# Performance work log

Hardware: AMD Instinct MI355X
Metric: run time of the kernel (lower is better)

Reference implementation:

```python
import jax, jax.numpy as jnp
import numpy as np

EMBED_DIM = 1024
N_TOKENS = 8192


def setup_inputs() -> dict:
    key = jax.random.key(0)
    kx, kr, ke = jax.random.split(key, 3)
    x = jax.random.normal(kx, (N_TOKENS, EMBED_DIM), dtype=jnp.float32)
    rotation_params = jax.random.normal(kr, (EMBED_DIM * EMBED_DIM,), dtype=jnp.float32) * 0.02
    entangle_params = jax.random.normal(ke, (EMBED_DIM * EMBED_DIM,), dtype=jnp.float32) * 0.02
    return {"x": x, "rotation_params": rotation_params, "entangle_params": entangle_params}


def reference(x, rotation_params, entangle_params):
    d = EMBED_DIM
    w_q = rotation_params.reshape(d, d)
    w_k = entangle_params.reshape(d, d)
    q = x @ w_q                      # [N, D]
    k = x @ w_k                      # [N, D]
    v = x                            # v is the raw input (as in source)
    scale = 1.0 / np.sqrt(d).astype(np.float32)
    scores = jax.nn.softmax(jnp.einsum('nd,md->nm', q, k) * scale, axis=-1)  # [N, N]
    return scores @ v                # [N, D]
```

## Files before the change

### kernel.cpp

```cpp
#include <hip/hip_runtime.h>
#include <hip/hip_bf16.h>
#include <stdint.h>

#define EMBED 1024
#define NTOK 8192
#define QRANGE 4.5f

#define BUFB (48 * 1024)
#define SMEM_TOTAL (3 * BUFB)
#define BBUF (64 * 1024)
#define SMEM_BIG (2 * BBUF)

typedef short bf16x8 __attribute__((ext_vector_type(8)));
typedef float f32x4 __attribute__((ext_vector_type(4)));
typedef int int4v __attribute__((ext_vector_type(4)));

__device__ inline unsigned short f2bf(float f) {
    union { float f; unsigned u; } c; c.f = f;
    unsigned u = c.u;
    unsigned r = (u + 0x7fffu + ((u >> 16) & 1u)) >> 16;
    return (unsigned short)r;
}

__device__ __forceinline__ void bar_sync_drain() {
    asm volatile("s_waitcnt vmcnt(0)\n\ts_barrier" ::: "memory");
}
__device__ __forceinline__ void bar_sync_cnt6() {
    asm volatile("s_waitcnt vmcnt(6)\n\ts_barrier" ::: "memory");
}

__device__ inline void xcd_remap(int& bx, int& by) {
    if ((gridDim.y & 7) == 0) {
        int bid = by * gridDim.x + bx;
        by = bid % gridDim.y;
        bx = bid / gridDim.y;
    }
}

__global__ void prep_x(const float* __restrict__ x, unsigned short* __restrict__ xb,
                       unsigned short* __restrict__ xbT) {
    __shared__ unsigned short tile[32][33];
    int bj = blockIdx.x, bi = blockIdx.y;
    int tx = threadIdx.x, ty = threadIdx.y;
#pragma unroll
    for (int r = 0; r < 4; ++r) {
        int row = ty + r * 8;
        size_t gi = (size_t)(bi * 32 + row) * EMBED + bj * 32 + tx;
        unsigned short h = f2bf(x[gi]);
        xb[gi] = h;
        tile[row][tx] = h;
    }
    __syncthreads();
#pragma unroll
    for (int r = 0; r < 4; ++r) {
        int row = ty + r * 8;
        xbT[(size_t)(bj * 32 + row) * NTOK + bi * 32 + tx] = tile[tx][row];
    }
}

__global__ void prep_w2(const float* __restrict__ wq, const float* __restrict__ wk,
                        unsigned short* __restrict__ wT, float* __restrict__ Z) {
    if (blockIdx.z == 2) {
        if (blockIdx.x == 0 && blockIdx.y == 0) {
            int t = threadIdx.y * 32 + threadIdx.x;
            for (int i = t; i < NTOK; i += 256) Z[i] = 0.f;
        }
        return;
    }
    __shared__ unsigned short tile[32][33];
    int bj = blockIdx.x, bi = blockIdx.y;
    int tx = threadIdx.x, ty = threadIdx.y;
    const float* w = blockIdx.z ? wk : wq;
    unsigned short* dst = wT + (size_t)blockIdx.z * EMBED * EMBED;
#pragma unroll
    for (int r = 0; r < 4; ++r) {
        int row = ty + r * 8;
        tile[row][tx] = f2bf(w[(size_t)(bi * 32 + row) * EMBED + bj * 32 + tx]);
    }
    __syncthreads();
#pragma unroll
    for (int r = 0; r < 4; ++r) {
        int row = ty + r * 8;
        dst[(size_t)(bj * 32 + row) * EMBED + bi * 32 + tx] = tile[tx][row];
    }
}

template<int MODE> struct GAcc { using T = f32x4; };
template<> struct GAcc<1> { using T = int4v; };
template<int MODE> struct GFrag { using T = bf16x8; };
template<> struct GFrag<1> { using T = int4v; };

__device__ __forceinline__ void stage_rows(const char* __restrict__ G, char* dst,
                                           size_t base, int ld, int kB, int tid,
                                           int niter) {
    const int srow = tid >> 3;
    const int csw  = ((tid & 7) ^ (srow & 7)) << 4;
    const int dof  = srow * 128 + ((tid & 7) << 4);
    const char* g = G + (base + srow) * (size_t)ld + kB + csw;
    char* d = dst + dof;
    for (int it = 0; it < niter; ++it)
        __builtin_amdgcn_global_load_lds(
            (const __attribute__((address_space(1))) void*)(g + (size_t)it * 64 * ld),
            (__attribute__((address_space(3))) void*)(d + it * 64 * 128), 16, 0, 0);
}

__device__ __forceinline__ void stage256(const char* __restrict__ A,
                                         const char* __restrict__ B,
                                         char* dst, size_t aBase, size_t bBase,
                                         int ldA, int ldB, int kB, int tid) {
    stage_rows(A, dst, aBase, ldA, kB, tid, 4);
    stage_rows(B, dst + 32768, bBase, ldB, kB, tid, 2);
}

__device__ __forceinline__ void stage_big(const char* __restrict__ A,
                                          const char* __restrict__ B,
                                          char* dst, size_t aBase, size_t bBase,
                                          int ldA, int ldB, int kB, int tid) {
    stage_rows(A, dst, aBase, ldA, kB, tid, 4);
    stage_rows(B, dst + 32768, bBase, ldB, kB, tid, 4);
}

template<int MODE, int NF>
__device__ __forceinline__ void ld_fr(typename GFrag<MODE>::T (&fr)[NF],
                                      const char* S, int wbase, int l15, int quad,
                                      int s) {
    using FT = typename GFrag<MODE>::T;
    const int sl = ((((s << 2) + quad) ^ (l15 & 7)) << 4);
#pragma unroll
    for (int f = 0; f < NF; ++f)
        fr[f] = *(const FT*)(S + (wbase + f * 16 + l15) * 128 + sl);
}

template<int MODE, int MT, int NT>
__device__ __forceinline__ void mfma_mn(typename GAcc<MODE>::T (&acc)[MT][NT],
                                        typename GFrag<MODE>::T (&af)[MT],
                                        typename GFrag<MODE>::T (&bf)[NT]) {
#pragma unroll
    for (int mt = 0; mt < MT; ++mt)
#pragma unroll
        for (int nt = 0; nt < NT; ++nt) {
            if constexpr (MODE == 1)
                acc[mt][nt] = __builtin_amdgcn_mfma_i32_16x16x64_i8(
                    af[mt], bf[nt], acc[mt][nt], 0, 0, 0);
            else
                acc[mt][nt] = __builtin_amdgcn_mfma_f32_16x16x32_bf16(
                    af[mt], bf[nt], acc[mt][nt], 0, 0, 0);
        }
}

template<int MODE>
__global__ __launch_bounds__(512, 2) void gemm256(
    const char* __restrict__ A, const char* __restrict__ B, void* __restrict__ Cv,
    int KB, int ldA, int ldB, int ldC, float qsc,
    float* __restrict__ Z, int beta, const float* __restrict__ Zn)
{
    extern __shared__ char smem[];
    const int tid  = threadIdx.x;
    const int lane = tid & 63;
    const int wid  = tid >> 6;
    const int wm   = (wid >> 1) << 6;
    const int wn   = (wid & 1) << 6;
    const int quad = lane >> 4;
    const int l15  = lane & 15;

    int bx = blockIdx.x, by = blockIdx.y;
    xcd_remap(bx, by);
    const size_t mBase = (size_t)by * 256;
    const size_t nBase = (size_t)bx * 128;

    using FT = typename GFrag<MODE>::T;
    typename GAcc<MODE>::T acc[4][4] = {};
    FT a0[4], b0[4], a1[4], b1[4];

    const int nsteps = KB >> 7;
    stage256(A, B, smem, mBase, nBase, ldA, ldB, 0, tid);
    if (nsteps > 1) {
        stage256(A, B, smem + BUFB, mBase, nBase, ldA, ldB, 128, tid);
        bar_sync_cnt6();
    } else {
        bar_sync_drain();
    }
    __builtin_amdgcn_sched_barrier(0);
    ld_fr<MODE, 4>(a0, smem, wm, l15, quad, 0);
    ld_fr<MODE, 4>(b0, smem + 32768, wn, l15, quad, 0);

    int bc = 0;
    for (int t = 0; t < nsteps; ++t) {
        const char* As = smem + bc * BUFB;
        ld_fr<MODE, 4>(a1, As, wm, l15, quad, 1);
        ld_fr<MODE, 4>(b1, As + 32768, wn, l15, quad, 1);
        __builtin_amdgcn_s_setprio(1);
        mfma_mn<MODE, 4, 4>(acc, a0, b0);
        __builtin_amdgcn_s_setprio(0);
        if (t + 1 < nsteps) {
            bar_sync_drain();
            __builtin_amdgcn_sched_barrier(0);
            int bn = bc + 1; if (bn >= 3) bn -= 3;
            const char* An = smem + bn * BUFB;
            ld_fr<MODE, 4>(a0, An, wm, l15, quad, 0);
            ld_fr<MODE, 4>(b0, An + 32768, wn, l15, quad, 0);
            if (t + 2 < nsteps) {
                int bs = bc + 2; if (bs >= 3) bs -= 3;
                stage256(A, B, smem + bs * BUFB, mBase, nBase, ldA, ldB,
                         (t + 2) << 7, tid);
            }
        }
        __builtin_amdgcn_s_setprio(1);
        mfma_mn<MODE, 4, 4>(acc, a1, b1);
        __builtin_amdgcn_s_setprio(0);
        ++bc; if (bc >= 3) bc -= 3;
    }
    __syncthreads();

    if constexpr (MODE == 2) {
        float* stf = (float*)smem + wid * (16 * 68);
        float* C = (float*)Cv;
#pragma unroll
        for (int mt = 0; mt < 4; ++mt) {
#pragma unroll
            for (int nt = 0; nt < 4; ++nt) {
                f32x4 v = acc[mt][nt];
#pragma unroll
                for (int r = 0; r < 4; ++r)
                    stf[(quad * 4 + r) * 68 + nt * 16 + l15] = v[r];
            }
#pragma unroll
            for (int pass = 0; pass < 4; ++pass) {
                int row = pass * 4 + (lane >> 4);
                int cc  = (lane & 15) * 4;
                f32x4 vv = *(const f32x4*)(stf + row * 68 + cc);
                size_t grow = mBase + wm + mt * 16 + row;
                float* gp = C + grow * (size_t)ldC + nBase + wn + cc;
                if (beta) {
                    f32x4 old = *(const f32x4*)gp;
                    vv = vv + old;
                }
                if (Zn) {
                    float inv = 1.0f / Zn[grow];
                    vv = vv * inv;
                }
                *(f32x4*)gp = vv;
            }
        }
    }
}

template<int MODE>
__global__ __launch_bounds__(512, 2) void gemmBig(
    const char* __restrict__ A, const char* __restrict__ B, void* __restrict__ Cv,
    int KB, int ldA, int ldB, int ldC, float qsc, float* __restrict__ Z)
{
    extern __shared__ char smem[];
    const int tid  = threadIdx.x;
    const int lane = tid & 63;
    const int wid  = tid >> 6;
    const int wm   = (wid >> 2) << 7;
    const int wn   = (wid & 3) << 6;
    const int quad = lane >> 4;
    const int l15  = lane & 15;

    int bx = blockIdx.x, by = blockIdx.y;
    xcd_remap(bx, by);
    const size_t mBase = (size_t)by * 256;
    const size_t nBase = (size_t)bx * 256;

    using FT = typename GFrag<MODE>::T;
    typename GAcc<MODE>::T acc[8][4] = {};
    FT af[8], bf[4];

    const int nsteps = KB >> 7;
    stage_big(A, B, smem, mBase, nBase, ldA, ldB, 0, tid);

    for (int t = 0; t < nsteps; ++t) {
        bar_sync_drain();
        __builtin_amdgcn_sched_barrier(0);
        if (t + 1 < nsteps)
            stage_big(A, B, smem + ((t + 1) & 1) * BBUF, mBase, nBase, ldA, ldB,
                      (t + 1) << 7, tid);
        const char* As = smem + (t & 1) * BBUF;
        const char* Bs = As + 32768;
#pragma unroll
        for (int s = 0; s < 2; ++s) {
            ld_fr<MODE, 8>(af, As, wm, l15, quad, s);
            ld_fr<MODE, 4>(bf, Bs, wn, l15, quad, s);
            __builtin_amdgcn_s_setprio(1);
            mfma_mn<MODE, 8, 4>(acc, af, bf);
            __builtin_amdgcn_s_setprio(0);
        }
    }
    __syncthreads();

    if constexpr (MODE == 0) {
        float* stf = (float*)smem + wid * (16 * 68);
        unsigned char* C = (unsigned char*)Cv;
        const float qinv = 127.0f / QRANGE;
#pragma unroll
        for (int mt = 0; mt < 8; ++mt) {
#pragma unroll
            for (int nt = 0; nt < 4; ++nt) {
                f32x4 v = acc[mt][nt];
#pragma unroll
                for (int r = 0; r < 4; ++r)
                    stf[(quad * 4 + r) * 68 + nt * 16 + l15] = v[r];
            }
#pragma unroll
            for (int pass = 0; pass < 4; ++pass) {
                int row = pass * 4 + (lane >> 4);
                int cc  = (lane & 15) * 4;
                f32x4 vv = *(const f32x4*)(stf + row * 68 + cc);
                int b[4];
#pragma unroll
                for (int r = 0; r < 4; ++r)
                    b[r] = __float2int_rn(fminf(fmaxf(vv[r] * qinv, -127.f), 127.f));
                int pk = (b[0] & 0xff) | ((b[1] & 0xff) << 8) |
                         ((b[2] & 0xff) << 16) | (b[3] << 24);
                size_t grow = mBase + wm + mt * 16 + row;
                *(int*)(C + grow * (size_t)ldC + nBase + wn + cc) = pk;
            }
        }
    } else {
        unsigned short* st = (unsigned short*)smem + wid * (16 * 72);
        unsigned short* C = (unsigned short*)Cv;
#pragma unroll
        for (int mt = 0; mt < 8; ++mt) {
            float rs[4] = {0.f, 0.f, 0.f, 0.f};
#pragma unroll
            for (int nt = 0; nt < 4; ++nt) {
                int4v v = acc[mt][nt];
#pragma unroll
                for (int r = 0; r < 4; ++r) {
                    float e = __expf((float)v[r] * qsc);
                    rs[r] += e;
                    st[(quad * 4 + r) * 72 + nt * 16 + l15] = f2bf(e);
                }
            }
#pragma unroll
            for (int r = 0; r < 4; ++r) {
                float s = rs[r];
                s += __shfl_xor(s, 1);
                s += __shfl_xor(s, 2);
                s += __shfl_xor(s, 4);
                s += __shfl_xor(s, 8);
                if (l15 == 0)
                    atomicAdd(&Z[mBase + wm + mt * 16 + quad * 4 + r], s);
            }
#pragma unroll
            for (int pass = 0; pass < 2; ++pass) {
                int row = pass * 8 + (lane >> 3);
                int cc  = (lane & 7) * 8;
                bf16x8 vv = *(const bf16x8*)(st + row * 72 + cc);
                size_t grow = mBase + wm + mt * 16 + row;
                *(bf16x8*)(C + grow * (size_t)ldC + nBase + wn + cc) = vv;
            }
        }
    }
}

extern "C" void kernel_launch(void* const* d_in, const int* in_sizes, int n_in,
                              void* d_out, int out_size, void* d_ws, size_t ws_size,
                              hipStream_t stream) {
    const float* x  = (const float*)d_in[0];
    const float* wq = (const float*)d_in[1];
    const float* wk = (const float*)d_in[2];
    float* out = (float*)d_out;

    char* p = (char*)d_ws;
    unsigned short* xb   = (unsigned short*)p; p += (size_t)NTOK * EMBED * 2;
    unsigned short* xbT  = (unsigned short*)p; p += (size_t)NTOK * EMBED * 2;
    signed char*    qk8  = (signed char*)p;    p += (size_t)NTOK * 2 * EMBED;
    unsigned short* wqkT = (unsigned short*)p; p += (size_t)2 * EMBED * EMBED * 2;
    float* Z = (float*)p; p += (size_t)NTOK * 4;
    unsigned short* P = (unsigned short*)p;

    size_t used  = (size_t)(p - (char*)d_ws);
    size_t avail = ws_size > used ? (ws_size - used) / 2 : 0;
    int NC = NTOK;
    while (NC > 256 && (size_t)NTOK * NC > avail) NC >>= 1;

    hipFuncSetAttribute((const void*)gemm256<2>,
                        hipFuncAttributeMaxDynamicSharedMemorySize, SMEM_TOTAL);
    hipFuncSetAttribute((const void*)gemmBig<0>,
                        hipFuncAttributeMaxDynamicSharedMemorySize, SMEM_BIG);
    hipFuncSetAttribute((const void*)gemmBig<1>,
                        hipFuncAttributeMaxDynamicSharedMemorySize, SMEM_BIG);

    prep_x<<<dim3(EMBED / 32, NTOK / 32), dim3(32, 8), 0, stream>>>(x, xb, xbT);
    prep_w2<<<dim3(32, 32, 3), dim3(32, 8), 0, stream>>>(wq, wk, wqkT, Z);

    gemmBig<0><<<dim3(2 * EMBED / 256, NTOK / 256), 512, SMEM_BIG, stream>>>(
        (const char*)xb, (const char*)wqkT, qk8,
        2 * EMBED, 2 * EMBED, 2 * EMBED, 2 * EMBED,
        0.f, nullptr);

    const char* q8 = (const char*)qk8;
    const char* k8 = q8 + EMBED;
    const float qsc = (QRANGE / 127.0f) * (QRANGE / 127.0f) / 32.0f;
    for (int c0 = 0; c0 < NTOK; c0 += NC) {
        const bool last = (c0 + NC >= NTOK);
        gemmBig<1><<<dim3(NC / 256, NTOK / 256), 512, SMEM_BIG, stream>>>(
            q8, k8 + (size_t)c0 * 2 * EMBED, P,
            EMBED, 2 * EMBED, 2 * EMBED, NC,
            qsc, Z);
        gemm256<2><<<dim3(EMBED / 128, NTOK / 256), 512, SMEM_TOTAL, stream>>>(
            (const char*)P, (const char*)(xbT + c0), out,
            NC * 2, NC * 2, NTOK * 2, EMBED,
            0.f, nullptr, c0 > 0 ? 1 : 0, last ? Z : nullptr);
    }
}
```

Before: 338.0 us.

## Quantize softmax probabilities and V to int8 for the PV GEMM

The second GEMM (P @ V) now runs on int8 MFMA instead of bf16. The unnormalized exp scores are stored as int8 centered at PMAX/2, V is stored transposed as int8, and a per-column V rowsum correction restores the offset in the epilogue. This halves the P and V traffic and uses the faster int8 matrix instructions. The cost is much coarser quantization of probabilities, which are clamped at PMAX, so accuracy may drift.

```diff
diff --git a/kernel.cpp b/kernel.cpp
--- a/kernel.cpp
+++ b/kernel.cpp
@@ -4,7 +4,10 @@
 
 #define EMBED 1024
 #define NTOK 8192
-#define QRANGE 4.5f
+#define XR 4.5f
+#define QKR 3.8f
+#define PMAX 14.0f
+#define PC (PMAX * 0.5f)
 
 #define BUFB (48 * 1024)
 #define SMEM_TOTAL (3 * BUFB)
@@ -38,23 +41,25 @@
 }
 
 __global__ void prep_x(const float* __restrict__ x, unsigned short* __restrict__ xb,
-                       unsigned short* __restrict__ xbT) {
-    __shared__ unsigned short tile[32][33];
+                       signed char* __restrict__ x8T) {
+    __shared__ signed char tile8[32][33];
     int bj = blockIdx.x, bi = blockIdx.y;
     int tx = threadIdx.x, ty = threadIdx.y;
+    const float qinv = 127.0f / XR;
 #pragma unroll
     for (int r = 0; r < 4; ++r) {
         int row = ty + r * 8;
         size_t gi = (size_t)(bi * 32 + row) * EMBED + bj * 32 + tx;
-        unsigned short h = f2bf(x[gi]);
-        xb[gi] = h;
-        tile[row][tx] = h;
+        float v = x[gi];
+        xb[gi] = f2bf(v);
+        tile8[row][tx] = (signed char)__float2int_rn(
+            fminf(fmaxf(v * qinv, -127.f), 127.f));
     }
     __syncthreads();
 #pragma unroll
     for (int r = 0; r < 4; ++r) {
         int row = ty + r * 8;
-        xbT[(size_t)(bj * 32 + row) * NTOK + bi * 32 + tx] = tile[tx][row];
+        x8T[(size_t)(bj * 32 + row) * NTOK + bi * 32 + tx] = tile8[tx][row];
     }
 }
 
@@ -85,10 +90,28 @@
     }
 }
 
+__global__ void rowsum8(const signed char* __restrict__ x8T, int* __restrict__ S8,
+                        int c0, int NC) {
+    int d = blockIdx.x * 4 + (threadIdx.x >> 6);
+    int lane = threadIdx.x & 63;
+    const signed char* r = x8T + (size_t)d * NTOK + c0;
+    int s = 0;
+    for (int i = lane * 4; i < NC; i += 256) {
+        int w = *(const int*)(r + i);
+        s += (int)(signed char)(w & 0xff) + (int)(signed char)((w >> 8) & 0xff)
+           + (int)(signed char)((w >> 16) & 0xff) + (int)(signed char)((w >> 24) & 0xff);
+    }
+    s += __shfl_xor(s, 1);  s += __shfl_xor(s, 2);  s += __shfl_xor(s, 4);
+    s += __shfl_xor(s, 8);  s += __shfl_xor(s, 16); s += __shfl_xor(s, 32);
+    if (lane == 0) S8[d] = s;
+}
+
 template<int MODE> struct GAcc { using T = f32x4; };
 template<> struct GAcc<1> { using T = int4v; };
+template<> struct GAcc<3> { using T = int4v; };
 template<int MODE> struct GFrag { using T = bf16x8; };
 template<> struct GFrag<1> { using T = int4v; };
+template<> struct GFrag<3> { using T = int4v; };
 
 __device__ __forceinline__ void stage_rows(const char* __restrict__ G, char* dst,
                                            size_t base, int ld, int kB, int tid,
@@ -139,7 +162,7 @@
     for (int mt = 0; mt < MT; ++mt)
 #pragma unroll
         for (int nt = 0; nt < NT; ++nt) {
-            if constexpr (MODE == 1)
+            if constexpr (MODE == 1 || MODE == 3)
                 acc[mt][nt] = __builtin_amdgcn_mfma_i32_16x16x64_i8(
                     af[mt], bf[nt], acc[mt][nt], 0, 0, 0);
             else
@@ -152,7 +175,8 @@
 __global__ __launch_bounds__(512, 2) void gemm256(
     const char* __restrict__ A, const char* __restrict__ B, void* __restrict__ Cv,
     int KB, int ldA, int ldB, int ldC, float qsc,
-    float* __restrict__ Z, int beta, const float* __restrict__ Zn)
+    float* __restrict__ Z, int beta, const float* __restrict__ Zn,
+    const int* __restrict__ S8c, float ccoef)
 {
     extern __shared__ char smem[];
     const int tid  = threadIdx.x;
@@ -212,17 +236,28 @@
     }
     __syncthreads();
 
-    if constexpr (MODE == 2) {
+    if constexpr (MODE == 2 || MODE == 3) {
         float* stf = (float*)smem + wid * (16 * 68);
         float* C = (float*)Cv;
+        float scorr[4] = {0.f, 0.f, 0.f, 0.f};
+        if constexpr (MODE == 3) {
+#pragma unroll
+            for (int nt = 0; nt < 4; ++nt)
+                scorr[nt] = ccoef * (float)S8c[nBase + wn + nt * 16 + l15];
+        }
 #pragma unroll
         for (int mt = 0; mt < 4; ++mt) {
 #pragma unroll
             for (int nt = 0; nt < 4; ++nt) {
-                f32x4 v = acc[mt][nt];
-#pragma unroll
-                for (int r = 0; r < 4; ++r)
-                    stf[(quad * 4 + r) * 68 + nt * 16 + l15] = v[r];
+#pragma unroll
+                for (int r = 0; r < 4; ++r) {
+                    float fv;
+                    if constexpr (MODE == 3)
+                        fv = (float)acc[mt][nt][r] * qsc + scorr[nt];
+                    else
+                        fv = acc[mt][nt][r];
+                    stf[(quad * 4 + r) * 68 + nt * 16 + l15] = fv;
+                }
             }
 #pragma unroll
             for (int pass = 0; pass < 4; ++pass) {
@@ -293,7 +328,7 @@
     if constexpr (MODE == 0) {
         float* stf = (float*)smem + wid * (16 * 68);
         unsigned char* C = (unsigned char*)Cv;
-        const float qinv = 127.0f / QRANGE;
+        const float qinv = 127.0f / QKR;
 #pragma unroll
         for (int mt = 0; mt < 8; ++mt) {
 #pragma unroll
@@ -319,8 +354,9 @@
             }
         }
     } else {
-        unsigned short* st = (unsigned short*)smem + wid * (16 * 72);
-        unsigned short* C = (unsigned short*)Cv;
+        float* stf = (float*)smem + wid * (16 * 68);
+        unsigned char* C = (unsigned char*)Cv;
+        const float qinv = 254.0f / PMAX;
 #pragma unroll
         for (int mt = 0; mt < 8; ++mt) {
             float rs[4] = {0.f, 0.f, 0.f, 0.f};
@@ -331,7 +367,7 @@
                 for (int r = 0; r < 4; ++r) {
                     float e = __expf((float)v[r] * qsc);
                     rs[r] += e;
-                    st[(quad * 4 + r) * 72 + nt * 16 + l15] = f2bf(e);
+                    stf[(quad * 4 + r) * 68 + nt * 16 + l15] = e;
                 }
             }
 #pragma unroll
@@ -345,12 +381,19 @@
                     atomicAdd(&Z[mBase + wm + mt * 16 + quad * 4 + r], s);
             }
 #pragma unroll
-            for (int pass = 0; pass < 2; ++pass) {
-                int row = pass * 8 + (lane >> 3);
-                int cc  = (lane & 7) * 8;
-                bf16x8 vv = *(const bf16x8*)(st + row * 72 + cc);
+            for (int pass = 0; pass < 4; ++pass) {
+                int row = pass * 4 + (lane >> 4);
+                int cc  = (lane & 15) * 4;
+                f32x4 vv = *(const f32x4*)(stf + row * 68 + cc);
+                int b[4];
+#pragma unroll
+                for (int r = 0; r < 4; ++r)
+                    b[r] = __float2int_rn(
+                        fminf(fmaxf((vv[r] - PC) * qinv, -127.f), 127.f));
+                int pk = (b[0] & 0xff) | ((b[1] & 0xff) << 8) |
+                         ((b[2] & 0xff) << 16) | (b[3] << 24);
                 size_t grow = mBase + wm + mt * 16 + row;
-                *(bf16x8*)(C + grow * (size_t)ldC + nBase + wn + cc) = vv;
+                *(int*)(C + grow * (size_t)ldC + nBase + wn + cc) = pk;
             }
         }
     }
@@ -366,25 +409,26 @@
 
     char* p = (char*)d_ws;
     unsigned short* xb   = (unsigned short*)p; p += (size_t)NTOK * EMBED * 2;
-    unsigned short* xbT  = (unsigned short*)p; p += (size_t)NTOK * EMBED * 2;
+    signed char*    x8T  = (signed char*)p;    p += (size_t)EMBED * NTOK;
     signed char*    qk8  = (signed char*)p;    p += (size_t)NTOK * 2 * EMBED;
     unsigned short* wqkT = (unsigned short*)p; p += (size_t)2 * EMBED * EMBED * 2;
     float* Z = (float*)p; p += (size_t)NTOK * 4;
-    unsigned short* P = (unsigned short*)p;
+    int*   S8 = (int*)p;  p += (size_t)EMBED * 4;
+    signed char* P = (signed char*)p;
 
     size_t used  = (size_t)(p - (char*)d_ws);
-    size_t avail = ws_size > used ? (ws_size - used) / 2 : 0;
+    size_t avail = ws_size > used ? (ws_size - used) : 0;
     int NC = NTOK;
     while (NC > 256 && (size_t)NTOK * NC > avail) NC >>= 1;
 
-    hipFuncSetAttribute((const void*)gemm256<2>,
+    hipFuncSetAttribute((const void*)gemm256<3>,
                         hipFuncAttributeMaxDynamicSharedMemorySize, SMEM_TOTAL);
     hipFuncSetAttribute((const void*)gemmBig<0>,
                         hipFuncAttributeMaxDynamicSharedMemorySize, SMEM_BIG);
     hipFuncSetAttribute((const void*)gemmBig<1>,
                         hipFuncAttributeMaxDynamicSharedMemorySize, SMEM_BIG);
 
-    prep_x<<<dim3(EMBED / 32, NTOK / 32), dim3(32, 8), 0, stream>>>(x, xb, xbT);
+    prep_x<<<dim3(EMBED / 32, NTOK / 32), dim3(32, 8), 0, stream>>>(x, xb, x8T);
     prep_w2<<<dim3(32, 32, 3), dim3(32, 8), 0, stream>>>(wq, wk, wqkT, Z);
 
     gemmBig<0><<<dim3(2 * EMBED / 256, NTOK / 256), 512, SMEM_BIG, stream>>>(
@@ -394,16 +438,20 @@
 
     const char* q8 = (const char*)qk8;
     const char* k8 = q8 + EMBED;
-    const float qsc = (QRANGE / 127.0f) * (QRANGE / 127.0f) / 32.0f;
+    const float qsc = (QKR / 127.0f) * (QKR / 127.0f) / 32.0f;
+    const float xstep = XR / 127.0f;
+    const float qsc2 = (PMAX / 254.0f) * xstep;
+    const float ccoef = PC * xstep;
     for (int c0 = 0; c0 < NTOK; c0 += NC) {
         const bool last = (c0 + NC >= NTOK);
         gemmBig<1><<<dim3(NC / 256, NTOK / 256), 512, SMEM_BIG, stream>>>(
             q8, k8 + (size_t)c0 * 2 * EMBED, P,
             EMBED, 2 * EMBED, 2 * EMBED, NC,
             qsc, Z);
-        gemm256<2><<<dim3(EMBED / 128, NTOK / 256), 512, SMEM_TOTAL, stream>>>(
-            (const char*)P, (const char*)(xbT + c0), out,
-            NC * 2, NC * 2, NTOK * 2, EMBED,
-            0.f, nullptr, c0 > 0 ? 1 : 0, last ? Z : nullptr);
-    }
-}
+        rowsum8<<<dim3(EMBED / 4), 256, 0, stream>>>(x8T, S8, c0, NC);
+        gemm256<3><<<dim3(EMBED / 128, NTOK / 256), 512, SMEM_TOTAL, stream>>>(
+            (const char*)P, (const char*)(x8T + c0), out,
+            NC, NC, NTOK, EMBED,
+            qsc2, nullptr, c0 > 0 ? 1 : 0, last ? Z : nullptr, S8, ccoef);
+    }
+}
```

Result: faster. 285.4 us (-15.6%).
